# Optimization experiments

Measured on AMD Instinct MI355X. Metric: run time of the kernel, lower is better.

Reference implementation:

```python
import jax, jax.numpy as jnp
import numpy as np

H = 1536
NH = 24
HD = 64
B = 2
S = 2048


def _rotate_half(x):
    x1, x2 = x[..., : HD // 2], x[..., HD // 2 :]
    return jnp.concatenate((-x2, x1), axis=-1)


def setup_inputs() -> dict:
    key = jax.random.key(0)
    ks = jax.random.split(key, 8)
    scale = 1.0 / np.sqrt(H)
    pos = jnp.arange(S)[:, None]
    inv_freq = 1.0 / (10000.0 ** (jnp.arange(0, HD, 2, dtype=jnp.float32) / HD))
    ang = pos * inv_freq[None, :]
    ang = jnp.concatenate([ang, ang], axis=-1)  # [S, HD]
    return {
        "hidden_states": jax.random.normal(ks[0], (B, S, H), jnp.float32),
        "rope_cos": jnp.cos(ang),
        "rope_sin": jnp.sin(ang),
        "wq": jax.random.normal(ks[1], (H, H), jnp.float32) * scale,
        "bq": jnp.zeros((H,), jnp.float32),
        "wk": jax.random.normal(ks[2], (H, H), jnp.float32) * scale,
        "bk": jnp.zeros((H,), jnp.float32),
        "wv": jax.random.normal(ks[3], (H, H), jnp.float32) * scale,
        "bv": jnp.zeros((H,), jnp.float32),
        "wo": jax.random.normal(ks[4], (H, H), jnp.float32) * scale,
        "bo": jnp.zeros((H,), jnp.float32),
    }


def reference(hidden_states, rope_cos, rope_sin, wq, bq, wk, bk, wv, bv, wo, bo):
    b, s, _ = hidden_states.shape
    # QKV projections (torch Linear: x @ W.T + b)
    q = hidden_states @ wq.T + bq
    k = hidden_states @ wk.T + bk
    v = hidden_states @ wv.T + bv
    # [B, NH, S, HD]
    q = q.reshape(b, s, NH, HD).transpose(0, 2, 1, 3)
    k = k.reshape(b, s, NH, HD).transpose(0, 2, 1, 3)
    v = v.reshape(b, s, NH, HD).transpose(0, 2, 1, 3)
    # RoPE: cos/sin broadcast over batch & heads
    cos = rope_cos[None, None, :, :]
    sin = rope_sin[None, None, :, :]
    q = q * cos + _rotate_half(q) * sin
    k = k * cos + _rotate_half(k) * sin
    # SDPA
    scores = jnp.einsum("bhqd,bhkd->bhqk", q, k) / jnp.sqrt(jnp.float32(HD))
    attn = jax.nn.softmax(scores, axis=-1)
    out = jnp.einsum("bhqk,bhkd->bhqd", attn, v)
    out = out.transpose(0, 2, 1, 3).reshape(b, s, NH * HD)
    return out @ wo.T + bo
```

## Files before the change

### kernel.cpp

```cpp
#include <hip/hip_runtime.h>
#include <hip/hip_bf16.h>
#include <cstdint>

namespace {
constexpr int H_  = 1536;
constexpr int NH_ = 24;
constexpr int HD_ = 64;
constexpr int B_  = 2;
constexpr int S_  = 2048;
constexpr int M_  = B_ * S_;
constexpr int KD_ = H_;
}

typedef __attribute__((ext_vector_type(8)))  short bf16x8;
typedef __attribute__((ext_vector_type(4)))  float f32x4;
typedef __attribute__((ext_vector_type(16))) float f32x16;

__device__ __forceinline__ unsigned short f2bf_fast(float x) {
    return (unsigned short)((__float_as_uint(x) + 0x8000u) >> 16);
}
__device__ __forceinline__ unsigned pack2bf(float b_hi, float a_lo) {
    const unsigned ub = __float_as_uint(b_hi) + 0x8000u;
    const unsigned ua = __float_as_uint(a_lo) + 0x8000u;
    return (ub & 0xffff0000u) | (ua >> 16);
}
__device__ __forceinline__ unsigned cvt_pk_bf16(float lo, float hi) {
    unsigned r;
    asm("v_cvt_pk_bf16_f32 %0, %1, %2" : "=v"(r) : "v"(lo), "v"(hi));
    return r;
}

__device__ __forceinline__ float fast_exp2(float x) {
#if __has_builtin(__builtin_amdgcn_exp2f)
    return __builtin_amdgcn_exp2f(x);
#else
    return exp2f(x);
#endif
}

__device__ __forceinline__ void gload16(const short* g, short* l) {
    __builtin_amdgcn_global_load_lds(
        (const __attribute__((address_space(1))) unsigned int*)g,
        (__attribute__((address_space(3))) unsigned int*)l, 16, 0, 0);
}

__global__ __launch_bounds__(256)
void cast_all(const float* __restrict__ X,
              const float* __restrict__ wq, const float* __restrict__ wk,
              const float* __restrict__ wv, const float* __restrict__ wo,
              short* __restrict__ Xh,
              short* __restrict__ Wqh, short* __restrict__ Wkh,
              short* __restrict__ Wvh, short* __restrict__ Woh)
{
    constexpr int XB = (M_*H_) / 1024;
    constexpr int WB = (H_*H_) / 1024;
    const int bid = blockIdx.x;
    const float* src; short* dst; int off;
    if (bid < XB)            { src = X;  dst = Xh;  off = bid; }
    else {
        const int r = bid - XB, wsel = r / WB; off = r % WB;
        if      (wsel == 0)  { src = wq; dst = Wqh; }
        else if (wsel == 1)  { src = wk; dst = Wkh; }
        else if (wsel == 2)  { src = wv; dst = Wvh; }
        else                 { src = wo; dst = Woh; }
    }
    const int i = (off * 256 + threadIdx.x) * 4;
    const float4 v = *(const float4*)&src[i];
    uint2 o;
    o.x = pack2bf(v.y, v.x);
    o.y = pack2bf(v.w, v.z);
    *(uint2*)&dst[i] = o;
}

template<int KIND>
__global__ __launch_bounds__(256, 4)
void gemm_bf16(const short* __restrict__ A_g,
               const short* __restrict__ Wq, const short* __restrict__ Wk,
               const short* __restrict__ Wv,
               const float* __restrict__ bq, const float* __restrict__ bk,
               const float* __restrict__ bv,
               const float* __restrict__ cosb, const float* __restrict__ sinb,
               short* __restrict__ Qb, short* __restrict__ Kb,
               short* __restrict__ Vt, float* __restrict__ outf)
{
    __shared__ short Ah[128*64], Bh[128*64];

    const int t    = threadIdx.x;
    const int lane = t & 63;
    const int w    = t >> 6;
    const int wr   = w >> 1, wc = w & 1;
    const int l15  = lane & 15;
    const int grp  = lane >> 4;

    const int xcd = blockIdx.x & 7;
    const int off = blockIdx.x >> 3;
    const int m_idx = xcd * 4 + (off & 3);
    const int rest  = off >> 2;
    const int n_idx = rest % 12;
    const int zi    = (KIND == 0) ? rest / 12 : 3;

    const int m0 = m_idx * 128;
    const int n0 = n_idx * 128;

    const short* bhg; const float* bias;
    if (KIND == 0) {
        if      (zi == 0) { bhg = Wq; bias = bq; }
        else if (zi == 1) { bhg = Wk; bias = bk; }
        else              { bhg = Wv; bias = bv; }
    } else {
        bhg = Wq; bias = bq;
    }

    f32x4 acc[4][4];
#pragma unroll
    for (int i = 0; i < 4; ++i)
#pragma unroll
        for (int j = 0; j < 4; ++j) acc[i][j] = (f32x4){0.f, 0.f, 0.f, 0.f};

    const int srow  = lane >> 3;
    const int sslot = (lane & 7) ^ srow;

    for (int kt = 0; kt < KD_; kt += 64) {
        __syncthreads();
#pragma unroll
        for (int cc = 0; cc < 4; ++cc) {
            const int c = w * 4 + cc;
            const int r = c * 8 + srow;
            gload16(A_g + (size_t)(m0 + r) * KD_ + kt + sslot * 8, Ah + c * 512);
            gload16(bhg + (size_t)(n0 + r) * KD_ + kt + sslot * 8, Bh + c * 512);
        }
        __syncthreads();

#pragma unroll
        for (int kk = 0; kk < 2; ++kk) {
            bf16x8 af[4], bfr[4];
#pragma unroll
            for (int i = 0; i < 4; ++i) {
                const int ra = wr * 64 + i * 16 + l15;
                af[i]  = *(const bf16x8*)&Ah[ra * 64 + (((kk*4 + grp) ^ (ra & 7)) << 3)];
                const int rb = wc * 64 + i * 16 + l15;
                bfr[i] = *(const bf16x8*)&Bh[rb * 64 + (((kk*4 + grp) ^ (rb & 7)) << 3)];
            }
#pragma unroll
            for (int i = 0; i < 4; ++i)
#pragma unroll
                for (int j = 0; j < 4; ++j)
                    acc[i][j] = __builtin_amdgcn_mfma_f32_16x16x32_bf16(af[i], bfr[j], acc[i][j], 0, 0, 0);
        }
    }

    float bn[4];
#pragma unroll
    for (int ni = 0; ni < 4; ++ni) bn[ni] = bias[n0 + wc * 64 + ni * 16 + l15];
    const int hw = (n0 + wc * 64) >> 6;

    if (KIND == 1) {
#pragma unroll
        for (int mi = 0; mi < 4; ++mi)
#pragma unroll
            for (int r = 0; r < 4; ++r) {
                const int m = m0 + wr * 64 + mi * 16 + grp * 4 + r;
#pragma unroll
                for (int ni = 0; ni < 4; ++ni)
                    outf[(size_t)m * H_ + n0 + wc * 64 + ni * 16 + l15] =
                        acc[mi][ni][r] + bn[ni];
            }
        return;
    }

    if (zi == 2) {
        const int b = m0 >> 11;
#pragma unroll
        for (int mi = 0; mi < 4; ++mi) {
            const int sb = (m0 & (S_ - 1)) + wr * 64 + mi * 16 + grp * 4;
#pragma unroll
            for (int ni = 0; ni < 4; ++ni) {
                const int d = ni * 16 + l15;
                uint2 o;
                o.x = pack2bf(acc[mi][ni][1] + bn[ni], acc[mi][ni][0] + bn[ni]);
                o.y = pack2bf(acc[mi][ni][3] + bn[ni], acc[mi][ni][2] + bn[ni]);
                *(uint2*)&Vt[((size_t)(b * NH_ + hw) * HD_ + d) * S_ + sb] = o;
            }
        }
        return;
    }

    const float sc = (zi == 0) ? 0.18033688011112042f : 1.0f;
    short* dst = (zi == 0) ? Qb : Kb;
#pragma unroll
    for (int mi = 0; mi < 4; ++mi)
#pragma unroll
        for (int r = 0; r < 4; ++r) {
            const int m = m0 + wr * 64 + mi * 16 + grp * 4 + r;
            const int b = m >> 11;
            const int s = m & (S_ - 1);
#pragma unroll
            for (int ni = 0; ni < 4; ++ni) {
                const int d  = ni * 16 + l15;
                const float val = acc[mi][ni][r] + bn[ni];
                const float pv  = acc[mi][ni ^ 2][r] + bn[ni ^ 2];
                const float cs = cosb[s * HD_ + d];
                const float sn = sinb[s * HD_ + d];
                const float rot = (ni < 2) ? -pv : pv;
                dst[((size_t)(b * NH_ + hw) * S_ + s) * HD_ + d] =
                    (short)f2bf_fast((val * cs + rot * sn) * sc);
            }
        }
}

__global__ __launch_bounds__(256, 3)
void attn_mfma(const short* __restrict__ Q, const short* __restrict__ K,
               const short* __restrict__ Vt, short* __restrict__ AO)
{
    __shared__ short Ks[2][4096];
    __shared__ short Vs[2][4096];

    const int t    = threadIdx.x;
    const int lane = t & 63;
    const int wid  = t >> 6;

    const int bid = blockIdx.x;
    const int xcd = bid & 7;
    const int sq  = bid >> 3;
    const int bh  = xcd * 6 + (sq >> 4);
    const int q0  = (sq & 15) * 128;

    const int l31 = lane & 31;
    const int hi  = lane >> 5;
    const int sw7 = lane & 7;

    const short* Qg = Q  + ((size_t)bh * S_ + q0 + wid*32) * HD_;
    const short* Kg = K  + (size_t)bh * S_ * HD_;
    const short* Vg = Vt + (size_t)bh * HD_ * S_;

    bf16x8 qf[4];
#pragma unroll
    for (int kk = 0; kk < 4; ++kk)
        qf[kk] = *(const bf16x8*)(Qg + (size_t)l31*HD_ + kk*16 + hi*8);

    f32x16 oacc[2];
#pragma unroll
    for (int nt = 0; nt < 2; ++nt)
#pragma unroll
        for (int r = 0; r < 16; ++r) oacc[nt][r] = 0.f;
    float la[4] = {0.f, 0.f, 0.f, 0.f};

    auto stageKV = [&](int b, int kt) {
#pragma unroll
        for (int cc = 0; cc < 2; ++cc) {
            const int d   = cc * 256 + t;
            const int row = d >> 3;
            const int sg  = (d & 7) ^ (row & 7);
            gload16(Kg + (size_t)(kt + row) * HD_ + sg * 8, &Ks[b][d * 8]);
            gload16(Vg + (size_t)row * S_ + kt + sg * 8,    &Vs[b][d * 8]);
        }
    };

    stageKV(0, 0);
    __syncthreads();
    int cur = 0;

    for (int kt = 0; kt < S_; kt += 64) {
        if (kt + 64 < S_) stageKV(cur ^ 1, kt + 64);

        f32x16 sac[2];
#pragma unroll
        for (int nt = 0; nt < 2; ++nt)
#pragma unroll
            for (int r = 0; r < 16; ++r) sac[nt][r] = 0.f;
        __builtin_amdgcn_s_setprio(1);
#pragma unroll
        for (int kk = 0; kk < 4; ++kk) {
#pragma unroll
            for (int nt = 0; nt < 2; ++nt) {
                const int row = nt*32 + l31;
                const bf16x8 kfrag = *(const bf16x8*)
                    &Ks[cur][row*64 + (((kk*2 + hi) ^ sw7) << 3)];
                sac[nt] = __builtin_amdgcn_mfma_f32_32x32x16_bf16(kfrag, qf[kk], sac[nt], 0, 0, 0);
            }
        }
        __builtin_amdgcn_s_setprio(0);

#pragma unroll
        for (int nt = 0; nt < 2; ++nt)
#pragma unroll
            for (int r = 0; r < 16; ++r) {
                sac[nt][r] = fast_exp2(sac[nt][r]);
                la[r & 3] += sac[nt][r];
            }

        unsigned pw[4][4];
#pragma unroll
        for (int kk = 0; kk < 4; ++kk) {
            const int h  = kk >> 1;
            const int g2 = (kk & 1) * 2;
#pragma unroll
            for (int e = 0; e < 2; ++e) {
                unsigned A = cvt_pk_bf16(sac[h][4*g2     + 2*e], sac[h][4*g2     + 2*e + 1]);
                unsigned Bv= cvt_pk_bf16(sac[h][4*(g2+1) + 2*e], sac[h][4*(g2+1) + 2*e + 1]);
                asm volatile("v_permlane32_swap_b32 %0, %1" : "+v"(A), "+v"(Bv));
                pw[kk][e]     = A;
                pw[kk][e + 2] = Bv;
            }
        }

        __builtin_amdgcn_s_setprio(1);
#pragma unroll
        for (int ks = 0; ks < 4; ++ks) {
            union { unsigned u[4]; bf16x8 v; } pf;
            pf.u[0] = pw[ks][0]; pf.u[1] = pw[ks][1];
            pf.u[2] = pw[ks][2]; pf.u[3] = pw[ks][3];
#pragma unroll
            for (int nt = 0; nt < 2; ++nt) {
                const int row = nt*32 + l31;
                const bf16x8 vfrag = *(const bf16x8*)
                    &Vs[cur][row*64 + (((ks*2 + hi) ^ sw7) << 3)];
                oacc[nt] = __builtin_amdgcn_mfma_f32_32x32x16_bf16(vfrag, pf.v, oacc[nt], 0, 0, 0);
            }
        }
        __builtin_amdgcn_s_setprio(0);

        __syncthreads();
        cur ^= 1;
    }

    float lacc = (la[0] + la[1]) + (la[2] + la[3]);
    lacc += __shfl_xor(lacc, 32);
    const float inv = 1.f / lacc;

    const int b = bh / NH_, h = bh % NH_;
    const int srow = q0 + wid*32 + l31;
    const size_t rowb = ((size_t)(b*S_ + srow)) * H_ + h*HD_;
#pragma unroll
    for (int nt = 0; nt < 2; ++nt)
#pragma unroll
        for (int i = 0; i < 8; ++i) {
            const int crow = ((2*i) & 3) + 8*((2*i) >> 2) + 4*hi;
            const int d    = nt*32 + crow;
            *(unsigned*)&AO[rowb + d] =
                cvt_pk_bf16(oacc[nt][2*i]*inv, oacc[nt][2*i+1]*inv);
        }
}

extern "C" void kernel_launch(void* const* d_in, const int* in_sizes, int n_in,
                              void* d_out, int out_size, void* d_ws, size_t ws_size,
                              hipStream_t stream)
{
    const float* X    = (const float*)d_in[0];
    const float* cosb = (const float*)d_in[1];
    const float* sinb = (const float*)d_in[2];
    const float* wq   = (const float*)d_in[3];
    const float* bq   = (const float*)d_in[4];
    const float* wk   = (const float*)d_in[5];
    const float* bk   = (const float*)d_in[6];
    const float* wv   = (const float*)d_in[7];
    const float* bv   = (const float*)d_in[8];
    const float* wo   = (const float*)d_in[9];
    const float* bo   = (const float*)d_in[10];
    float* out = (float*)d_out;

    const size_t MH = (size_t)M_ * H_;
    const size_t HH = (size_t)H_ * H_;

    short* Xh  = (short*)d_ws;
    short* Wqh = Xh  + MH;
    short* Wkh = Wqh + HH;
    short* Wvh = Wkh + HH;
    short* Woh = Wvh + HH;
    short* Qb  = Woh + HH;
    short* Kb  = Qb + MH;
    short* Vt  = Kb + MH;
    short* AO  = Vt + MH;

    cast_all<<<(int)(MH/1024 + 4*(HH/1024)), 256, 0, stream>>>(
        X, wq, wk, wv, wo, Xh, Wqh, Wkh, Wvh, Woh);

    gemm_bf16<0><<<1152, 256, 0, stream>>>(Xh, Wqh, Wkh, Wvh,
        bq, bk, bv, cosb, sinb, Qb, Kb, Vt, nullptr);

    attn_mfma<<<768, 256, 0, stream>>>(Qb, Kb, Vt, AO);

    gemm_bf16<1><<<384, 256, 0, stream>>>(AO, Woh, nullptr, nullptr,
        bo, nullptr, nullptr, nullptr, nullptr, nullptr, nullptr, nullptr, out);
}
```

Before: 184.2 us.

## Software-pipeline attention loop: overlap next-tile QK^T with softmax and PV

```diff
diff --git a/kernel.cpp b/kernel.cpp
--- a/kernel.cpp
+++ b/kernel.cpp
@@ -208,12 +208,12 @@
         }
 }
 
-__global__ __launch_bounds__(256, 3)
+__global__ __launch_bounds__(256, 2)
 void attn_mfma(const short* __restrict__ Q, const short* __restrict__ K,
                const short* __restrict__ Vt, short* __restrict__ AO)
 {
-    __shared__ short Ks[2][4096];
-    __shared__ short Vs[2][4096];
+    __shared__ short Ks[3][4096];
+    __shared__ short Vs[3][4096];
 
     const int t    = threadIdx.x;
     const int lane = t & 63;
@@ -256,18 +256,9 @@
         }
     };
 
-    stageKV(0, 0);
-    __syncthreads();
-    int cur = 0;
-
-    for (int kt = 0; kt < S_; kt += 64) {
-        if (kt + 64 < S_) stageKV(cur ^ 1, kt + 64);
-
-        f32x16 sac[2];
-#pragma unroll
-        for (int nt = 0; nt < 2; ++nt)
-#pragma unroll
-            for (int r = 0; r < 16; ++r) sac[nt][r] = 0.f;
+    auto qkt = [&](int cb, f32x16* sac) {
+        sac[0] = (f32x16)(0.f);
+        sac[1] = (f32x16)(0.f);
         __builtin_amdgcn_s_setprio(1);
 #pragma unroll
         for (int kk = 0; kk < 4; ++kk) {
@@ -275,12 +266,14 @@
             for (int nt = 0; nt < 2; ++nt) {
                 const int row = nt*32 + l31;
                 const bf16x8 kfrag = *(const bf16x8*)
-                    &Ks[cur][row*64 + (((kk*2 + hi) ^ sw7) << 3)];
+                    &Ks[cb][row*64 + (((kk*2 + hi) ^ sw7) << 3)];
                 sac[nt] = __builtin_amdgcn_mfma_f32_32x32x16_bf16(kfrag, qf[kk], sac[nt], 0, 0, 0);
             }
         }
         __builtin_amdgcn_s_setprio(0);
-
+    };
+
+    auto sm_pack = [&](f32x16* sac, unsigned (&pw)[4][4]) {
 #pragma unroll
         for (int nt = 0; nt < 2; ++nt)
 #pragma unroll
@@ -288,8 +281,6 @@
                 sac[nt][r] = fast_exp2(sac[nt][r]);
                 la[r & 3] += sac[nt][r];
             }
-
-        unsigned pw[4][4];
 #pragma unroll
         for (int kk = 0; kk < 4; ++kk) {
             const int h  = kk >> 1;
@@ -303,7 +294,9 @@
                 pw[kk][e + 2] = Bv;
             }
         }
-
+    };
+
+    auto pv = [&](unsigned (&pw)[4][4], int vb) {
         __builtin_amdgcn_s_setprio(1);
 #pragma unroll
         for (int ks = 0; ks < 4; ++ks) {
@@ -314,15 +307,47 @@
             for (int nt = 0; nt < 2; ++nt) {
                 const int row = nt*32 + l31;
                 const bf16x8 vfrag = *(const bf16x8*)
-                    &Vs[cur][row*64 + (((ks*2 + hi) ^ sw7) << 3)];
+                    &Vs[vb][row*64 + (((ks*2 + hi) ^ sw7) << 3)];
                 oacc[nt] = __builtin_amdgcn_mfma_f32_32x32x16_bf16(vfrag, pf.v, oacc[nt], 0, 0, 0);
             }
         }
         __builtin_amdgcn_s_setprio(0);
-
-        __syncthreads();
-        cur ^= 1;
-    }
+    };
+
+    stageKV(0, 0);
+    stageKV(1, 64);
+    __syncthreads();
+
+    f32x16 sacA[2], sacB[2];
+    unsigned pw[4][4];
+    qkt(0, sacA);
+
+    for (int tp = 1; tp + 1 < 32; tp += 2) {
+        {
+            const int cb = tp % 3, pb = (tp - 1) % 3, nb = (tp + 1) % 3;
+            qkt(cb, sacB);
+            stageKV(nb, (tp + 1) * 64);
+            sm_pack(sacA, pw);
+            pv(pw, pb);
+            __syncthreads();
+        }
+        {
+            const int t2 = tp + 1;
+            const int cb = t2 % 3, pb = (t2 - 1) % 3, nb = (t2 + 1) % 3;
+            qkt(cb, sacA);
+            stageKV(nb, (t2 + 1) * 64);
+            sm_pack(sacB, pw);
+            pv(pw, pb);
+            __syncthreads();
+        }
+    }
+    {
+        qkt(31 % 3, sacB);
+        sm_pack(sacA, pw);
+        pv(pw, 30 % 3);
+    }
+    sm_pack(sacB, pw);
+    pv(pw, 31 % 3);
 
     float lacc = (la[0] + la[1]) + (la[2] + la[3]);
     lacc += __shfl_xor(lacc, 32);
```

New measurement: 181.1 us, median of 2. About the same (-1.7%).
